# Kernel tuning notes

Measured on AMD Instinct MI355X. Metric: run time of the kernel, lower is better.

## Reference

```python
import jax, jax.numpy as jnp
import numpy as np

N_NODES = 50000
N_EDGES = 600000
D_IN = 128
D_HID = 128
NUM_LAYERS = 4


def setup_inputs() -> dict:
    key = jax.random.key(0)
    ks = jax.random.split(key, 8)
    x = jax.random.normal(ks[0], (N_NODES, D_IN), dtype=jnp.float32)
    edge_index = jax.random.randint(ks[1], (2, N_EDGES), 0, N_NODES, dtype=jnp.int32)
    s = 0.05
    # first_conv: lin_rel (weight+bias) applied to aggregated neighbors, lin_root (no bias) applied to x
    W1 = jax.random.normal(ks[2], (D_IN, D_HID), dtype=jnp.float32) * s
    b1 = jnp.zeros((D_HID,), dtype=jnp.float32)
    R1 = jax.random.normal(ks[3], (D_IN, D_HID), dtype=jnp.float32) * s
    # shared conv used for layers 2..NUM_LAYERS
    W2 = jax.random.normal(ks[4], (D_HID, D_HID), dtype=jnp.float32) * s
    b2 = jnp.zeros((D_HID,), dtype=jnp.float32)
    R2 = jax.random.normal(ks[5], (D_HID, D_HID), dtype=jnp.float32) * s
    return {"x": x, "edge_index": edge_index, "W1": W1, "b1": b1, "R1": R1,
            "W2": W2, "b2": b2, "R2": R2}


def _graph_conv(x, src, dst, W, b, R, num_nodes):
    # gather source features, scatter-max into destinations (PyG GraphConv, aggr='max')
    agg = jax.ops.segment_max(x[src], dst, num_segments=num_nodes)  # [N, d]
    agg = jnp.where(jnp.isneginf(agg), 0.0, agg)  # isolated nodes -> 0 (PyG fill)
    return agg @ W + b + x @ R  # lin_rel(agg) + lin_root(x)


def reference(x, edge_index, W1, b1, R1, W2, b2, R2):
    src, dst = edge_index[0], edge_index[1]
    n = x.shape[0]
    h = jax.nn.relu(_graph_conv(x, src, dst, W1, b1, R1, n))
    for _ in range(NUM_LAYERS - 1):  # shared weights, per original module
        h = jax.nn.relu(_graph_conv(h, src, dst, W2, b2, R2, n))
    return h
```

## Files before the change

kernel.cpp:

```cpp
#include <hip/hip_runtime.h>
#include <math.h>

static constexpr int NNODES = 50000;
static constexpr int NEDGES = 600000;
static constexpr int D = 128;
static constexpr int NPART = (NNODES + 255) / 256;

typedef __attribute__((ext_vector_type(8))) short short8;
typedef __attribute__((ext_vector_type(4))) float f32x4;

static __device__ inline unsigned short f2bf_rne(float f) {
  unsigned u = __float_as_uint(f);
  unsigned r = (u + 0x7FFFu + ((u >> 16) & 1u)) >> 16;
  return (unsigned short)r;
}
static __device__ inline float bf2f(unsigned short s) {
  return __uint_as_float(((unsigned)s) << 16);
}


__global__ void count_kernel(const int* __restrict__ dst, int* __restrict__ cnt, int nE) {
  int i = blockIdx.x * blockDim.x + threadIdx.x;
  if (i < nE) atomicAdd(&cnt[dst[i]], 1);
}

__global__ void scan_partial(const int* __restrict__ cnt, int* __restrict__ part, int n) {
  int i = blockIdx.x * 256 + threadIdx.x;
  int v = (i < n) ? cnt[i] : 0;
#pragma unroll
  for (int off = 32; off > 0; off >>= 1) v += __shfl_down(v, off);
  __shared__ int ws[4];
  int wid = threadIdx.x >> 6, lane = threadIdx.x & 63;
  if (lane == 0) ws[wid] = v;
  __syncthreads();
  if (threadIdx.x == 0) part[blockIdx.x] = ws[0] + ws[1] + ws[2] + ws[3];
}

__global__ void scan_root(const int* __restrict__ part, int* __restrict__ pscan,
                          int* __restrict__ rs_last, int np) {
  int i = threadIdx.x;
  int v = (i < np) ? part[i] : 0;
  int incl = v;
  int lane = i & 63, wid = i >> 6;
#pragma unroll
  for (int off = 1; off < 64; off <<= 1) {
    int t = __shfl_up(incl, off);
    if (lane >= off) incl += t;
  }
  __shared__ int ws[4];
  if (lane == 63) ws[wid] = incl;
  __syncthreads();
  int woff = 0;
  for (int w = 0; w < wid; ++w) woff += ws[w];
  if (i < np) pscan[i] = woff + incl - v;
  if (i == 0) *rs_last = ws[0] + ws[1] + ws[2] + ws[3];
}

__global__ void scan_apply(const int* __restrict__ cnt, const int* __restrict__ pscan,
                           int* __restrict__ rs, int* __restrict__ cursor, int n) {
  int i = blockIdx.x * 256 + threadIdx.x;
  int v = (i < n) ? cnt[i] : 0;
  int incl = v;
  int lane = threadIdx.x & 63, wid = threadIdx.x >> 6;
#pragma unroll
  for (int off = 1; off < 64; off <<= 1) {
    int t = __shfl_up(incl, off);
    if (lane >= off) incl += t;
  }
  __shared__ int ws[4];
  if (lane == 63) ws[wid] = incl;
  __syncthreads();
  int woff = pscan[blockIdx.x];
  for (int w = 0; w < wid; ++w) woff += ws[w];
  int ex = woff + incl - v;
  if (i < n) { rs[i] = ex; cursor[i] = ex; }
}

__global__ void fill_kernel(const int* __restrict__ src, const int* __restrict__ dst,
                            int* __restrict__ cursor, int* __restrict__ csr, int nE) {
  int i = blockIdx.x * blockDim.x + threadIdx.x;
  if (i < nE) {
    int d = dst[i];
    int p = atomicAdd(&cursor[d], 1);
    csr[p] = src[i];
  }
}

__global__ __launch_bounds__(256) void agg_kernel(const float* __restrict__ x,
    const int* __restrict__ rs, const int* __restrict__ csr,
    float* __restrict__ agg, int n) {
  int gw = (int)((blockIdx.x * blockDim.x + threadIdx.x) >> 6);
  int lane = threadIdx.x & 63;
  if (gw >= n) return;
  int beg = rs[gw], end = rs[gw + 1];
  const float2* xx = (const float2*)x;
  float2 acc;
  acc.x = -INFINITY; acc.y = -INFINITY;
  int j = beg;
  for (; j + 8 <= end; j += 8) {
    int s[8];
#pragma unroll
    for (int u = 0; u < 8; ++u) s[u] = csr[j + u];
    float2 v[8];
#pragma unroll
    for (int u = 0; u < 8; ++u) v[u] = xx[s[u] * 64 + lane];
#pragma unroll
    for (int u = 0; u < 8; ++u) {
      acc.x = fmaxf(acc.x, v[u].x);
      acc.y = fmaxf(acc.y, v[u].y);
    }
  }
  for (; j + 2 <= end; j += 2) {
    int s0 = csr[j], s1 = csr[j + 1];
    float2 v0 = xx[s0 * 64 + lane];
    float2 v1 = xx[s1 * 64 + lane];
    acc.x = fmaxf(acc.x, fmaxf(v0.x, v1.x));
    acc.y = fmaxf(acc.y, fmaxf(v0.y, v1.y));
  }
  for (; j < end; ++j) {
    int s = csr[j];
    float2 v = xx[s * 64 + lane];
    acc.x = fmaxf(acc.x, v.x);
    acc.y = fmaxf(acc.y, v.y);
  }
  if (beg == end) { acc.x = 0.f; acc.y = 0.f; }
  ((float2*)agg)[gw * 64 + lane] = acc;
}

struct PackArgs {
  const float* src[4];
  unsigned short* hi[4];
  unsigned short* lo[4];
};

__global__ void pack_all(PackArgs pa) {
  int mat = blockIdx.x >> 3;
  int tid = (blockIdx.x & 7) * 256 + threadIdx.x;
  const float* Wm = pa.src[mat];
  unsigned short* hi = pa.hi[mat];
  unsigned short* lo = pa.lo[mat];
  int jb = tid >> 8;
  int ks = (tid >> 6) & 3;
  int lane = tid & 63;
  int j = jb * 16 + (lane & 15);
  int k0 = ks * 32 + (lane >> 4) * 8;
#pragma unroll
  for (int e = 0; e < 8; ++e) {
    float v = Wm[(k0 + e) * D + j];
    unsigned short h = f2bf_rne(v);
    float rem = v - bf2f(h);
    unsigned short l = f2bf_rne(rem);
    hi[tid * 8 + e] = h;
    lo[tid * 8 + e] = l;
  }
}

__global__ __launch_bounds__(256) void gemm_mfma(
    const float* __restrict__ agg, const float* __restrict__ hin,
    const unsigned short* __restrict__ Whi, const unsigned short* __restrict__ Wlo,
    const unsigned short* __restrict__ Rhi, const unsigned short* __restrict__ Rlo,
    const float* __restrict__ bias, float* __restrict__ out, int nrows) {
  const int lane = threadIdx.x & 63;
  const int wv = threadIdx.x >> 6;
  const int m_lo = lane & 15;
  const int kgrp = lane >> 4;
  const int r_base = blockIdx.x * 128 + wv * 32;

  f32x4 acc[2][8];
#pragma unroll
  for (int g = 0; g < 2; ++g)
#pragma unroll
    for (int jb = 0; jb < 8; ++jb) acc[g][jb] = (f32x4)0.f;

  float bv[8];
#pragma unroll
  for (int jb = 0; jb < 8; ++jb) bv[jb] = bias[jb * 16 + m_lo];

  for (int ks = 0; ks < 4; ++ks) {
    short8 fa_hi[2], fa_lo[2], fh_hi[2], fh_lo[2];
#pragma unroll
    for (int g = 0; g < 2; ++g) {
      int row = r_base + g * 16 + m_lo;
      if (row >= nrows) row = nrows - 1;
      const float* ap = agg + (size_t)row * D + ks * 32 + kgrp * 8;
      const float* hp = hin + (size_t)row * D + ks * 32 + kgrp * 8;
      float av[8], hv[8];
      *(f32x4*)&av[0] = *(const f32x4*)(ap);
      *(f32x4*)&av[4] = *(const f32x4*)(ap + 4);
      *(f32x4*)&hv[0] = *(const f32x4*)(hp);
      *(f32x4*)&hv[4] = *(const f32x4*)(hp + 4);
#pragma unroll
      for (int e = 0; e < 8; ++e) {
        unsigned short h1 = f2bf_rne(av[e]);
        fa_hi[g][e] = (short)h1;
        fa_lo[g][e] = (short)f2bf_rne(av[e] - bf2f(h1));
        unsigned short h2 = f2bf_rne(hv[e]);
        fh_hi[g][e] = (short)h2;
        fh_lo[g][e] = (short)f2bf_rne(hv[e] - bf2f(h2));
      }
    }
#pragma unroll
    for (int jb = 0; jb < 8; ++jb) {
      const int pidx = ((jb * 4 + ks) * 64 + lane) * 8;
      short8 bwhi = *(const short8*)(Whi + pidx);
      short8 bwlo = *(const short8*)(Wlo + pidx);
      short8 brhi = *(const short8*)(Rhi + pidx);
      short8 brlo = *(const short8*)(Rlo + pidx);
#pragma unroll
      for (int g = 0; g < 2; ++g) {
        acc[g][jb] = __builtin_amdgcn_mfma_f32_16x16x32_bf16(fa_hi[g], bwhi, acc[g][jb], 0, 0, 0);
        acc[g][jb] = __builtin_amdgcn_mfma_f32_16x16x32_bf16(fa_lo[g], bwhi, acc[g][jb], 0, 0, 0);
        acc[g][jb] = __builtin_amdgcn_mfma_f32_16x16x32_bf16(fa_hi[g], bwlo, acc[g][jb], 0, 0, 0);
        acc[g][jb] = __builtin_amdgcn_mfma_f32_16x16x32_bf16(fh_hi[g], brhi, acc[g][jb], 0, 0, 0);
        acc[g][jb] = __builtin_amdgcn_mfma_f32_16x16x32_bf16(fh_lo[g], brhi, acc[g][jb], 0, 0, 0);
        acc[g][jb] = __builtin_amdgcn_mfma_f32_16x16x32_bf16(fh_hi[g], brlo, acc[g][jb], 0, 0, 0);
      }
    }
  }

#pragma unroll
  for (int g = 0; g < 2; ++g) {
#pragma unroll
    for (int jb = 0; jb < 8; ++jb) {
#pragma unroll
      for (int r = 0; r < 4; ++r) {
        int row = r_base + g * 16 + kgrp * 4 + r;
        if (row < nrows) {
          float v = acc[g][jb][r] + bv[jb];
          out[(size_t)row * D + jb * 16 + m_lo] = fmaxf(v, 0.f);
        }
      }
    }
  }
}


extern "C" void kernel_launch(void* const* d_in, const int* in_sizes, int n_in,
                              void* d_out, int out_size, void* d_ws, size_t ws_size,
                              hipStream_t stream) {
  const float* x  = (const float*)d_in[0];
  const int*   ei = (const int*)d_in[1];
  const float* W1 = (const float*)d_in[2];
  const float* b1 = (const float*)d_in[3];
  const float* R1 = (const float*)d_in[4];
  const float* W2 = (const float*)d_in[5];
  const float* b2 = (const float*)d_in[6];
  const float* R2 = (const float*)d_in[7];
  float* out = (float*)d_out;

  const int* src = ei;
  const int* dst = ei + NEDGES;

  char* ws = (char*)d_ws;
  size_t off = 0;
  auto alloc = [&](size_t bytes) -> void* {
    off = (off + 511) & ~(size_t)511;
    void* p = ws + off;
    off += bytes;
    return p;
  };
  float* aggbuf = (float*)alloc(sizeof(float) * (size_t)NNODES * D);
  float* hbuf   = (float*)alloc(sizeof(float) * (size_t)NNODES * D);
  int* cnt      = (int*)alloc(sizeof(int) * NNODES);
  int* rs       = (int*)alloc(sizeof(int) * (NNODES + 1));
  int* cursor   = (int*)alloc(sizeof(int) * NNODES);
  int* csr      = (int*)alloc(sizeof(int) * NEDGES);
  int* part     = (int*)alloc(sizeof(int) * NPART);
  int* pscan    = (int*)alloc(sizeof(int) * NPART);
  const int PACKN = 2048 * 8;
  unsigned short* w1hi = (unsigned short*)alloc(sizeof(short) * PACKN);
  unsigned short* w1lo = (unsigned short*)alloc(sizeof(short) * PACKN);
  unsigned short* r1hi = (unsigned short*)alloc(sizeof(short) * PACKN);
  unsigned short* r1lo = (unsigned short*)alloc(sizeof(short) * PACKN);
  unsigned short* w2hi = (unsigned short*)alloc(sizeof(short) * PACKN);
  unsigned short* w2lo = (unsigned short*)alloc(sizeof(short) * PACKN);
  unsigned short* r2hi = (unsigned short*)alloc(sizeof(short) * PACKN);
  unsigned short* r2lo = (unsigned short*)alloc(sizeof(short) * PACKN);

  PackArgs pa;
  pa.src[0] = W1; pa.hi[0] = w1hi; pa.lo[0] = w1lo;
  pa.src[1] = R1; pa.hi[1] = r1hi; pa.lo[1] = r1lo;
  pa.src[2] = W2; pa.hi[2] = w2hi; pa.lo[2] = w2lo;
  pa.src[3] = R2; pa.hi[3] = r2hi; pa.lo[3] = r2lo;
  pack_all<<<32, 256, 0, stream>>>(pa);

  hipMemsetAsync(cnt, 0, sizeof(int) * NNODES, stream);
  count_kernel<<<(NEDGES + 255) / 256, 256, 0, stream>>>(dst, cnt, NEDGES);
  scan_partial<<<NPART, 256, 0, stream>>>(cnt, part, NNODES);
  scan_root<<<1, 256, 0, stream>>>(part, pscan, &rs[NNODES], NPART);
  scan_apply<<<NPART, 256, 0, stream>>>(cnt, pscan, rs, cursor, NNODES);
  fill_kernel<<<(NEDGES + 255) / 256, 256, 0, stream>>>(src, dst, cursor, csr, NEDGES);

  const int gemm_grid = (NNODES + 127) / 128;

  auto layer = [&](const float* hin,
                   const unsigned short* whi, const unsigned short* wlo,
                   const unsigned short* rhi, const unsigned short* rlo,
                   const float* b, float* hout) {
    agg_kernel<<<(NNODES + 3) / 4, 256, 0, stream>>>(hin, rs, csr, aggbuf, NNODES);
    gemm_mfma<<<gemm_grid, 256, 0, stream>>>(aggbuf, hin, whi, wlo, rhi, rlo, b, hout, NNODES);
  };

  layer(x,    w1hi, w1lo, r1hi, r1lo, b1, hbuf);
  layer(hbuf, w2hi, w2lo, r2hi, r2lo, b2, out);
  layer(out,  w2hi, w2lo, r2hi, r2lo, b2, hbuf);
  layer(hbuf, w2hi, w2lo, r2hi, r2lo, b2, out);
}
```

Baseline: 415.3 us.

## Store activations as split bf16 hi/lo and gather max over bf16 hi only

Activations are now stored as bf16 hi/lo pairs written by the GEMM epilogue, plus a one-time split kernel for the input. The aggregation gathers only the bf16 hi half, which halves the random-gather traffic and writes a bf16 aggregate, so the GEMM drops one MFMA per tile and skips the in-kernel fp32-to-bf16 splitting. The cost is lower precision for the aggregated neighbor features: the max is taken over bf16-rounded values, so the aggregate lacks the lo correction term and accuracy could fall below tolerance.

New measurement: 415.3 us. About the same (+0.0%).

```diff
diff --git a/kernel.cpp b/kernel.cpp
--- a/kernel.cpp
+++ b/kernel.cpp
@@ -16,6 +16,20 @@
 }
 static __device__ inline float bf2f(unsigned short s) {
   return __uint_as_float(((unsigned)s) << 16);
+}
+
+__global__ __launch_bounds__(256) void split_kernel(const float* __restrict__ x,
+    unsigned short* __restrict__ hi, unsigned short* __restrict__ lo, int n4) {
+  int i = blockIdx.x * 256 + threadIdx.x;
+  if (i >= n4) return;
+  f32x4 v = *(const f32x4*)(x + (size_t)i * 4);
+  ushort4 h, l;
+  h.x = f2bf_rne(v[0]); l.x = f2bf_rne(v[0] - bf2f(h.x));
+  h.y = f2bf_rne(v[1]); l.y = f2bf_rne(v[1] - bf2f(h.y));
+  h.z = f2bf_rne(v[2]); l.z = f2bf_rne(v[2] - bf2f(h.z));
+  h.w = f2bf_rne(v[3]); l.w = f2bf_rne(v[3] - bf2f(h.w));
+  *(ushort4*)(hi + (size_t)i * 4) = h;
+  *(ushort4*)(lo + (size_t)i * 4) = l;
 }
 
 
@@ -86,45 +100,36 @@
   }
 }
 
-__global__ __launch_bounds__(256) void agg_kernel(const float* __restrict__ x,
+__global__ __launch_bounds__(256) void agg_kernel(const unsigned int* __restrict__ xb,
     const int* __restrict__ rs, const int* __restrict__ csr,
-    float* __restrict__ agg, int n) {
+    unsigned int* __restrict__ aggb, int n) {
   int gw = (int)((blockIdx.x * blockDim.x + threadIdx.x) >> 6);
   int lane = threadIdx.x & 63;
   if (gw >= n) return;
   int beg = rs[gw], end = rs[gw + 1];
-  const float2* xx = (const float2*)x;
-  float2 acc;
-  acc.x = -INFINITY; acc.y = -INFINITY;
+  float ax = -INFINITY, ay = -INFINITY;
   int j = beg;
   for (; j + 8 <= end; j += 8) {
     int s[8];
 #pragma unroll
     for (int u = 0; u < 8; ++u) s[u] = csr[j + u];
-    float2 v[8];
-#pragma unroll
-    for (int u = 0; u < 8; ++u) v[u] = xx[s[u] * 64 + lane];
+    unsigned v[8];
+#pragma unroll
+    for (int u = 0; u < 8; ++u) v[u] = xb[(size_t)s[u] * 64 + lane];
 #pragma unroll
     for (int u = 0; u < 8; ++u) {
-      acc.x = fmaxf(acc.x, v[u].x);
-      acc.y = fmaxf(acc.y, v[u].y);
+      ax = fmaxf(ax, bf2f((unsigned short)(v[u] & 0xFFFFu)));
+      ay = fmaxf(ay, bf2f((unsigned short)(v[u] >> 16)));
     }
   }
-  for (; j + 2 <= end; j += 2) {
-    int s0 = csr[j], s1 = csr[j + 1];
-    float2 v0 = xx[s0 * 64 + lane];
-    float2 v1 = xx[s1 * 64 + lane];
-    acc.x = fmaxf(acc.x, fmaxf(v0.x, v1.x));
-    acc.y = fmaxf(acc.y, fmaxf(v0.y, v1.y));
-  }
   for (; j < end; ++j) {
-    int s = csr[j];
-    float2 v = xx[s * 64 + lane];
-    acc.x = fmaxf(acc.x, v.x);
-    acc.y = fmaxf(acc.y, v.y);
-  }
-  if (beg == end) { acc.x = 0.f; acc.y = 0.f; }
-  ((float2*)agg)[gw * 64 + lane] = acc;
+    unsigned v = xb[(size_t)csr[j] * 64 + lane];
+    ax = fmaxf(ax, bf2f((unsigned short)(v & 0xFFFFu)));
+    ay = fmaxf(ay, bf2f((unsigned short)(v >> 16)));
+  }
+  if (beg == end) { ax = 0.f; ay = 0.f; }
+  aggb[(size_t)gw * 64 + lane] =
+      (__float_as_uint(ax) >> 16) | (__float_as_uint(ay) & 0xFFFF0000u);
 }
 
 struct PackArgs {
@@ -156,10 +161,12 @@
 }
 
 __global__ __launch_bounds__(256) void gemm_mfma(
-    const float* __restrict__ agg, const float* __restrict__ hin,
+    const unsigned short* __restrict__ aggb,
+    const unsigned short* __restrict__ hhi, const unsigned short* __restrict__ hlo,
     const unsigned short* __restrict__ Whi, const unsigned short* __restrict__ Wlo,
     const unsigned short* __restrict__ Rhi, const unsigned short* __restrict__ Rlo,
-    const float* __restrict__ bias, float* __restrict__ out, int nrows) {
+    const float* __restrict__ bias, float* __restrict__ outf,
+    unsigned short* __restrict__ ohi, unsigned short* __restrict__ olo, int nrows) {
   const int lane = threadIdx.x & 63;
   const int wv = threadIdx.x >> 6;
   const int m_lo = lane & 15;
@@ -177,27 +184,15 @@
   for (int jb = 0; jb < 8; ++jb) bv[jb] = bias[jb * 16 + m_lo];
 
   for (int ks = 0; ks < 4; ++ks) {
-    short8 fa_hi[2], fa_lo[2], fh_hi[2], fh_lo[2];
+    short8 fa[2], fhh[2], fhl[2];
 #pragma unroll
     for (int g = 0; g < 2; ++g) {
       int row = r_base + g * 16 + m_lo;
       if (row >= nrows) row = nrows - 1;
-      const float* ap = agg + (size_t)row * D + ks * 32 + kgrp * 8;
-      const float* hp = hin + (size_t)row * D + ks * 32 + kgrp * 8;
-      float av[8], hv[8];
-      *(f32x4*)&av[0] = *(const f32x4*)(ap);
-      *(f32x4*)&av[4] = *(const f32x4*)(ap + 4);
-      *(f32x4*)&hv[0] = *(const f32x4*)(hp);
-      *(f32x4*)&hv[4] = *(const f32x4*)(hp + 4);
-#pragma unroll
-      for (int e = 0; e < 8; ++e) {
-        unsigned short h1 = f2bf_rne(av[e]);
-        fa_hi[g][e] = (short)h1;
-        fa_lo[g][e] = (short)f2bf_rne(av[e] - bf2f(h1));
-        unsigned short h2 = f2bf_rne(hv[e]);
-        fh_hi[g][e] = (short)h2;
-        fh_lo[g][e] = (short)f2bf_rne(hv[e] - bf2f(h2));
-      }
+      const size_t ro = (size_t)row * D + ks * 32 + kgrp * 8;
+      fa[g]  = *(const short8*)(aggb + ro);
+      fhh[g] = *(const short8*)(hhi + ro);
+      fhl[g] = *(const short8*)(hlo + ro);
     }
 #pragma unroll
     for (int jb = 0; jb < 8; ++jb) {
@@ -208,12 +203,11 @@
       short8 brlo = *(const short8*)(Rlo + pidx);
 #pragma unroll
       for (int g = 0; g < 2; ++g) {
-        acc[g][jb] = __builtin_amdgcn_mfma_f32_16x16x32_bf16(fa_hi[g], bwhi, acc[g][jb], 0, 0, 0);
-        acc[g][jb] = __builtin_amdgcn_mfma_f32_16x16x32_bf16(fa_lo[g], bwhi, acc[g][jb], 0, 0, 0);
-        acc[g][jb] = __builtin_amdgcn_mfma_f32_16x16x32_bf16(fa_hi[g], bwlo, acc[g][jb], 0, 0, 0);
-        acc[g][jb] = __builtin_amdgcn_mfma_f32_16x16x32_bf16(fh_hi[g], brhi, acc[g][jb], 0, 0, 0);
-        acc[g][jb] = __builtin_amdgcn_mfma_f32_16x16x32_bf16(fh_lo[g], brhi, acc[g][jb], 0, 0, 0);
-        acc[g][jb] = __builtin_amdgcn_mfma_f32_16x16x32_bf16(fh_hi[g], brlo, acc[g][jb], 0, 0, 0);
+        acc[g][jb] = __builtin_amdgcn_mfma_f32_16x16x32_bf16(fa[g],  bwhi, acc[g][jb], 0, 0, 0);
+        acc[g][jb] = __builtin_amdgcn_mfma_f32_16x16x32_bf16(fa[g],  bwlo, acc[g][jb], 0, 0, 0);
+        acc[g][jb] = __builtin_amdgcn_mfma_f32_16x16x32_bf16(fhh[g], brhi, acc[g][jb], 0, 0, 0);
+        acc[g][jb] = __builtin_amdgcn_mfma_f32_16x16x32_bf16(fhl[g], brhi, acc[g][jb], 0, 0, 0);
+        acc[g][jb] = __builtin_amdgcn_mfma_f32_16x16x32_bf16(fhh[g], brlo, acc[g][jb], 0, 0, 0);
       }
     }
   }
@@ -226,8 +220,15 @@
       for (int r = 0; r < 4; ++r) {
         int row = r_base + g * 16 + kgrp * 4 + r;
         if (row < nrows) {
-          float v = acc[g][jb][r] + bv[jb];
-          out[(size_t)row * D + jb * 16 + m_lo] = fmaxf(v, 0.f);
+          float v = fmaxf(acc[g][jb][r] + bv[jb], 0.f);
+          size_t o = (size_t)row * D + jb * 16 + m_lo;
+          if (outf) {
+            outf[o] = v;
+          } else {
+            unsigned short h = f2bf_rne(v);
+            ohi[o] = h;
+            olo[o] = f2bf_rne(v - bf2f(h));
+          }
         }
       }
     }
@@ -259,14 +260,20 @@
     off += bytes;
     return p;
   };
-  float* aggbuf = (float*)alloc(sizeof(float) * (size_t)NNODES * D);
-  float* hbuf   = (float*)alloc(sizeof(float) * (size_t)NNODES * D);
-  int* cnt      = (int*)alloc(sizeof(int) * NNODES);
-  int* rs       = (int*)alloc(sizeof(int) * (NNODES + 1));
-  int* cursor   = (int*)alloc(sizeof(int) * NNODES);
-  int* csr      = (int*)alloc(sizeof(int) * NEDGES);
-  int* part     = (int*)alloc(sizeof(int) * NPART);
-  int* pscan    = (int*)alloc(sizeof(int) * NPART);
+  const size_t NF = (size_t)NNODES * D;
+  unsigned short* xhi  = (unsigned short*)alloc(sizeof(short) * NF);
+  unsigned short* xlo  = (unsigned short*)alloc(sizeof(short) * NF);
+  unsigned short* hAhi = (unsigned short*)alloc(sizeof(short) * NF);
+  unsigned short* hAlo = (unsigned short*)alloc(sizeof(short) * NF);
+  unsigned short* hBhi = (unsigned short*)alloc(sizeof(short) * NF);
+  unsigned short* hBlo = (unsigned short*)alloc(sizeof(short) * NF);
+  unsigned short* aggb = (unsigned short*)alloc(sizeof(short) * NF);
+  int* cnt    = (int*)alloc(sizeof(int) * NNODES);
+  int* rs     = (int*)alloc(sizeof(int) * (NNODES + 1));
+  int* cursor = (int*)alloc(sizeof(int) * NNODES);
+  int* csr    = (int*)alloc(sizeof(int) * NEDGES);
+  int* part   = (int*)alloc(sizeof(int) * NPART);
+  int* pscan  = (int*)alloc(sizeof(int) * NPART);
   const int PACKN = 2048 * 8;
   unsigned short* w1hi = (unsigned short*)alloc(sizeof(short) * PACKN);
   unsigned short* w1lo = (unsigned short*)alloc(sizeof(short) * PACKN);
@@ -277,6 +284,8 @@
   unsigned short* r2hi = (unsigned short*)alloc(sizeof(short) * PACKN);
   unsigned short* r2lo = (unsigned short*)alloc(sizeof(short) * PACKN);
 
+  split_kernel<<<(int)(NF / 4 + 255) / 256, 256, 0, stream>>>(x, xhi, xlo, (int)(NF / 4));
+
   PackArgs pa;
   pa.src[0] = W1; pa.hi[0] = w1hi; pa.lo[0] = w1lo;
   pa.src[1] = R1; pa.hi[1] = r1hi; pa.lo[1] = r1lo;
@@ -293,16 +302,18 @@
 
   const int gemm_grid = (NNODES + 127) / 128;
 
-  auto layer = [&](const float* hin,
+  auto layer = [&](const unsigned short* hhi, const unsigned short* hlo,
                    const unsigned short* whi, const unsigned short* wlo,
                    const unsigned short* rhi, const unsigned short* rlo,
-                   const float* b, float* hout) {
-    agg_kernel<<<(NNODES + 3) / 4, 256, 0, stream>>>(hin, rs, csr, aggbuf, NNODES);
-    gemm_mfma<<<gemm_grid, 256, 0, stream>>>(aggbuf, hin, whi, wlo, rhi, rlo, b, hout, NNODES);
+                   const float* b, float* outf, unsigned short* ohi, unsigned short* olo) {
+    agg_kernel<<<(NNODES + 3) / 4, 256, 0, stream>>>(
+        (const unsigned int*)hhi, rs, csr, (unsigned int*)aggb, NNODES);
+    gemm_mfma<<<gemm_grid, 256, 0, stream>>>(aggb, hhi, hlo, whi, wlo, rhi, rlo,
+                                             b, outf, ohi, olo, NNODES);
   };
 
-  layer(x,    w1hi, w1lo, r1hi, r1lo, b1, hbuf);
-  layer(hbuf, w2hi, w2lo, r2hi, r2lo, b2, out);
-  layer(out,  w2hi, w2lo, r2hi, r2lo, b2, hbuf);
-  layer(hbuf, w2hi, w2lo, r2hi, r2lo, b2, out);
-}
+  layer(xhi,  xlo,  w1hi, w1lo, r1hi, r1lo, b1, nullptr, hAhi, hAlo);
+  layer(hAhi, hAlo, w2hi, w2lo, r2hi, r2lo, b2, nullptr, hBhi, hBlo);
+  layer(hBhi, hBlo, w2hi, w2lo, r2hi, r2lo, b2, nullptr, hAhi, hAlo);
+  layer(hAhi, hAlo, w2hi, w2lo, r2hi, r2lo, b2, out, nullptr, nullptr);
+}
```
